# Optimization experiments

Hardware: AMD Instinct MI355X
Metric: run time of the kernel (lower is better)

The kernel has to match this reference:

```python
import jax, jax.numpy as jnp
import numpy as np

B, C, H, W = 16, 512, 64, 64


def setup_inputs() -> dict:
    key = jax.random.key(0)
    ks = jax.random.split(key, 8)
    s = 1.0 / np.sqrt(C)  # fan-in scale like torch conv default
    return {
        "x": jax.random.normal(ks[0], (B, C, H, W), dtype=jnp.float32),
        "y": jax.random.normal(ks[1], (B, C), dtype=jnp.float32),
        "wq": jax.random.normal(ks[2], (C, C), dtype=jnp.float32) * s,
        "bq": jax.random.normal(ks[3], (C,), dtype=jnp.float32) * s,
        "wk": jax.random.normal(ks[4], (C, C), dtype=jnp.float32) * s,
        "bk": jax.random.normal(ks[5], (C,), dtype=jnp.float32) * s,
        "wv": jax.random.normal(ks[6], (C, C), dtype=jnp.float32) * s,
        "bv": jax.random.normal(ks[7], (C,), dtype=jnp.float32) * s,
        "gamma": jnp.ones((1,), dtype=jnp.float32),
    }


def _conv1x1_flat(inp_flat, w, b):
    # inp_flat: (B, C, N); 1x1 conv == per-pixel channel GEMM
    return jnp.einsum("oc,bcn->bon", w, inp_flat) + b[None, :, None]


def reference(x, y, wq, bq, wk, bk, wv, bv, gamma):
    b, c, h, w = x.shape
    n = h * w
    # align=True: y (B, C) broadcast to (B, C, H, W); flatten spatial dims
    y_flat = jnp.broadcast_to(y[:, :, None], (b, c, n))
    x_flat = x.reshape(b, c, n)
    # exchange=False: q = y, k = v = x
    pq = _conv1x1_flat(y_flat, wq, bq)          # (B, C, N)
    pk = _conv1x1_flat(x_flat, wk, bk)          # (B, C, N)
    pv = _conv1x1_flat(x_flat, wv, bv)          # (B, C, N)
    energy = jnp.einsum("bcn,bdn->bcd", pq, pk)  # (B, C, C) channel attention
    attn = jax.nn.softmax(energy, axis=-1)
    out = jnp.einsum("bcd,bdn->bcn", attn, pv)   # (B, C, N)
    out = out.reshape(b, c, h, w)
    return gamma * out + x
```

## Files before the change

### kernel.cpp

```cpp
#include <hip/hip_runtime.h>
#include <hip/hip_bf16.h>

#define Bn 16
#define Cn 512
#define Nn 4096

typedef unsigned short u16;
typedef __bf16 bf16x8 __attribute__((ext_vector_type(8)));
typedef float f32x4 __attribute__((ext_vector_type(4)));

__device__ __forceinline__ u16 f2bf(float f) {
    __hip_bfloat16 h = __float2bfloat16(f);
    return *reinterpret_cast<u16*>(&h);
}

__global__ __launch_bounds__(256) void k_transpose(
    const float* __restrict__ x, u16* __restrict__ xt, float* __restrict__ sxp)
{
    __shared__ float tile[64 * 65];
    const int b = blockIdx.z, c0 = blockIdx.y * 64, n0 = blockIdx.x * 64;
    const int t = threadIdx.x;
    const float* xb = x + ((size_t)(b * Cn + c0)) * Nn + n0;

    float part[4];
#pragma unroll
    for (int r = 0; r < 4; ++r) {
        int cl = (t >> 4) + r * 16;
        int nl = (t & 15) * 4;
        float4 v = *(const float4*)(xb + (size_t)cl * Nn + nl);
        float* tp = &tile[cl * 65 + nl];
        tp[0] = v.x; tp[1] = v.y; tp[2] = v.z; tp[3] = v.w;
        part[r] = (v.x + v.y) + (v.z + v.w);
    }
#pragma unroll
    for (int m = 1; m < 16; m <<= 1) {
#pragma unroll
        for (int r = 0; r < 4; ++r) part[r] += __shfl_xor(part[r], m);
    }
    if ((t & 15) == 0) {
#pragma unroll
        for (int r = 0; r < 4; ++r) {
            int cl = (t >> 4) + r * 16;
            sxp[(size_t)(b * Cn + c0 + cl) * 64 + blockIdx.x] = part[r];
        }
    }
    __syncthreads();
    u16* xtb = xt + ((size_t)(b * Nn + n0)) * Cn + c0;
#pragma unroll
    for (int r = 0; r < 4; ++r) {
        int nl = (t >> 4) + r * 16;
        int c4 = (t & 15) * 4;
        ushort4 h;
        h.x = f2bf(tile[(c4 + 0) * 65 + nl]);
        h.y = f2bf(tile[(c4 + 1) * 65 + nl]);
        h.z = f2bf(tile[(c4 + 2) * 65 + nl]);
        h.w = f2bf(tile[(c4 + 3) * 65 + nl]);
        *(ushort4*)(xtb + (size_t)nl * Cn + c4) = h;
    }
}

__global__ __launch_bounds__(256) void k_sxred(
    const float* __restrict__ sxp, float* __restrict__ sx)
{
    int i = blockIdx.x * 256 + threadIdx.x;
    const float* p = sxp + (size_t)i * 64;
    float s = 0.f;
#pragma unroll
    for (int j = 0; j < 64; ++j) s += p[j];
    sx[i] = s;
}

__global__ __launch_bounds__(256) void k_qk(
    const float* __restrict__ wq, const float* __restrict__ bq,
    const float* __restrict__ wk, const float* __restrict__ bk,
    const float* __restrict__ y, const float* __restrict__ sx,
    float* __restrict__ qy, float* __restrict__ sk)
{
    const int w = threadIdx.x >> 6, lane = threadIdx.x & 63;
    const int o = blockIdx.x * 4 + w;
    const int b = blockIdx.y;
    const int mode = blockIdx.z;
    const float* W = mode ? wk : wq;
    const float* vec = mode ? (sx + b * Cn) : (y + b * Cn);
    float sum = 0.f;
#pragma unroll
    for (int i = 0; i < 8; ++i) {
        int k2 = lane + i * 64;
        sum += W[(size_t)o * Cn + k2] * vec[k2];
    }
#pragma unroll
    for (int m = 1; m < 64; m <<= 1) sum += __shfl_xor(sum, m);
    if (lane == 0) {
        if (mode) sk[b * Cn + o] = sum + 4096.0f * bk[o];
        else      qy[b * Cn + o] = sum + bq[o];
    }
}

__global__ __launch_bounds__(256) void k_wvt(
    const float* __restrict__ wv, u16* __restrict__ wvt)
{
    int idx = blockIdx.x * 256 + threadIdx.x;
    int e = idx >> 9, d = idx & 511;
    wvt[idx] = f2bf(wv[(size_t)d * Cn + e]);
}

__global__ __launch_bounds__(256) void k_softmax(
    const float* __restrict__ qy, const float* __restrict__ sk,
    const float* __restrict__ bv, u16* __restrict__ attn,
    float* __restrict__ beff)
{
    __shared__ float red[4], red2[4], red3[4];
    const int b = blockIdx.x >> 9, c = blockIdx.x & 511;
    const int t = threadIdx.x;
    const float q = qy[b * Cn + c];
    const float l0 = q * sk[b * Cn + t];
    const float l1 = q * sk[b * Cn + t + 256];
    float mx = fmaxf(l0, l1);
#pragma unroll
    for (int m = 1; m < 64; m <<= 1) mx = fmaxf(mx, __shfl_xor(mx, m));
    if ((t & 63) == 0) red[t >> 6] = mx;
    __syncthreads();
    mx = fmaxf(fmaxf(red[0], red[1]), fmaxf(red[2], red[3]));
    const float e0 = __expf(l0 - mx), e1 = __expf(l1 - mx);
    float s = e0 + e1;
#pragma unroll
    for (int m = 1; m < 64; m <<= 1) s += __shfl_xor(s, m);
    if ((t & 63) == 0) red2[t >> 6] = s;
    __syncthreads();
    s = red2[0] + red2[1] + red2[2] + red2[3];
    const float inv = 1.0f / s;
    const float a0 = e0 * inv, a1 = e1 * inv;
    u16* arow = attn + ((size_t)(b * Cn + c)) * Cn;
    arow[t] = f2bf(a0);
    arow[t + 256] = f2bf(a1);
    float pb = a0 * bv[t] + a1 * bv[t + 256];
#pragma unroll
    for (int m = 1; m < 64; m <<= 1) pb += __shfl_xor(pb, m);
    if ((t & 63) == 0) red3[t >> 6] = pb;
    __syncthreads();
    if (t == 0) beff[b * Cn + c] = red3[0] + red3[1] + red3[2] + red3[3];
}

template <int FINAL>
__global__ __launch_bounds__(256) void k_gemm(
    const u16* __restrict__ A, size_t strideA,
    const u16* __restrict__ Bt, size_t strideB,
    int N,
    u16* __restrict__ outBf, size_t strideOb,
    float* __restrict__ outF,
    const float* __restrict__ xres,
    const float* __restrict__ beff,
    const float* __restrict__ gamma)
{
    constexpr int K = 512;
    __shared__ u16 la[128 * 32];
    __shared__ u16 lb[128 * 32];
    const int b = blockIdx.z;
    const int m0 = blockIdx.y * 128;
    const int n0 = blockIdx.x * 128;
    A  += (size_t)b * strideA;
    Bt += (size_t)b * strideB;
    const int t = threadIdx.x;
    const int lane = t & 63;
    const int w = t >> 6;
    const int wm = (w >> 1) * 64, wn = (w & 1) * 64;
    const int l15 = lane & 15, quad = lane >> 4;

    f32x4 acc[4][4];
#pragma unroll
    for (int i = 0; i < 4; ++i)
#pragma unroll
        for (int j = 0; j < 4; ++j)
            acc[i][j] = (f32x4){0.f, 0.f, 0.f, 0.f};

    const int srow = t >> 2;
    const int scol = (t & 3) * 8;

    for (int k0 = 0; k0 < K; k0 += 32) {
        __syncthreads();
        *(uint4*)&la[srow * 32 + scol] =
            *(const uint4*)(A + (size_t)(m0 + srow) * K + k0 + scol);
        *(uint4*)&la[(srow + 64) * 32 + scol] =
            *(const uint4*)(A + (size_t)(m0 + srow + 64) * K + k0 + scol);
        *(uint4*)&lb[srow * 32 + scol] =
            *(const uint4*)(Bt + (size_t)(n0 + srow) * K + k0 + scol);
        *(uint4*)&lb[(srow + 64) * 32 + scol] =
            *(const uint4*)(Bt + (size_t)(n0 + srow + 64) * K + k0 + scol);
        __syncthreads();

        bf16x8 af[4], bfr[4];
#pragma unroll
        for (int mi = 0; mi < 4; ++mi)
            af[mi] = *(const bf16x8*)&la[(wm + mi * 16 + l15) * 32 + quad * 8];
#pragma unroll
        for (int ni = 0; ni < 4; ++ni)
            bfr[ni] = *(const bf16x8*)&lb[(wn + ni * 16 + l15) * 32 + quad * 8];
#pragma unroll
        for (int mi = 0; mi < 4; ++mi)
#pragma unroll
            for (int ni = 0; ni < 4; ++ni)
                acc[mi][ni] = __builtin_amdgcn_mfma_f32_16x16x32_bf16(
                    af[mi], bfr[ni], acc[mi][ni], 0, 0, 0);
    }

    if (FINAL) {
        const float g = gamma[0];
#pragma unroll
        for (int mi = 0; mi < 4; ++mi) {
#pragma unroll
            for (int reg = 0; reg < 4; ++reg) {
                const int r = m0 + wm + mi * 16 + quad * 4 + reg;
                const float be = beff[b * Cn + r];
                const size_t base = ((size_t)(b * Cn + r)) * N;
#pragma unroll
                for (int ni = 0; ni < 4; ++ni) {
                    const int cidx = n0 + wn + ni * 16 + l15;
                    outF[base + cidx] = g * (acc[mi][ni][reg] + be) + xres[base + cidx];
                }
            }
        }
    } else {
#pragma unroll
        for (int mi = 0; mi < 4; ++mi) {
#pragma unroll
            for (int reg = 0; reg < 4; ++reg) {
                const int r = m0 + wm + mi * 16 + quad * 4 + reg;
                const size_t base = (size_t)b * strideOb + (size_t)r * N;
#pragma unroll
                for (int ni = 0; ni < 4; ++ni) {
                    const int cidx = n0 + wn + ni * 16 + l15;
                    outBf[base + cidx] = f2bf(acc[mi][ni][reg]);
                }
            }
        }
    }
}

extern "C" void kernel_launch(void* const* d_in, const int* in_sizes, int n_in,
                              void* d_out, int out_size, void* d_ws, size_t ws_size,
                              hipStream_t stream)
{
    const float* x     = (const float*)d_in[0];
    const float* y     = (const float*)d_in[1];
    const float* wq    = (const float*)d_in[2];
    const float* bq    = (const float*)d_in[3];
    const float* wk    = (const float*)d_in[4];
    const float* bk    = (const float*)d_in[5];
    const float* wv    = (const float*)d_in[6];
    const float* bv    = (const float*)d_in[7];
    const float* gamma = (const float*)d_in[8];
    float* out = (float*)d_out;

    char* ws = (char*)d_ws;
    u16*   xt   = (u16*)  (ws + 0);
    float* sxp  = (float*)(ws + 67108864);
    float* sx   = (float*)(ws + 69206016);
    float* qy   = (float*)(ws + 69238784);
    float* sk   = (float*)(ws + 69271552);
    float* beff = (float*)(ws + 69304320);
    u16*   attn = (u16*)  (ws + 69337088);
    u16*   wvt  = (u16*)  (ws + 77725696);
    u16*   weff = (u16*)  (ws + 78249984);

    k_transpose<<<dim3(64, 8, Bn), dim3(256), 0, stream>>>(x, xt, sxp);
    k_sxred<<<dim3(32), dim3(256), 0, stream>>>(sxp, sx);
    k_wvt<<<dim3(1024), dim3(256), 0, stream>>>(wv, wvt);
    k_qk<<<dim3(128, Bn, 2), dim3(256), 0, stream>>>(wq, bq, wk, bk, y, sx, qy, sk);
    k_softmax<<<dim3(Bn * Cn), dim3(256), 0, stream>>>(qy, sk, bv, attn, beff);
    k_gemm<0><<<dim3(4, 4, Bn), dim3(256), 0, stream>>>(
        attn, (size_t)Cn * Cn, wvt, (size_t)0, Cn,
        weff, (size_t)Cn * Cn, nullptr, nullptr, nullptr, nullptr);
    k_gemm<1><<<dim3(32, 4, Bn), dim3(256), 0, stream>>>(
        weff, (size_t)Cn * Cn, xt, (size_t)Nn * Cn, Nn,
        nullptr, (size_t)0, out, x, beff, gamma);
}
```

Before: 366.4 us.

## Use direct global-to-LDS loads in GEMM and widen transpose writes

GEMM tile staging now uses global_load_lds so each wave copies its 16-row slice of A and B straight into shared memory, with no register round trip. The x transpose handles 128 channels per block and writes 16-byte bf16 vectors. The wv transpose becomes an LDS-tiled, coalesced kernel, and the partial-sum reduction reads float4. Together these aim to cut load-issue overhead and uncoalesced memory traffic, at the cost of more LDS use per transpose block.

Result: no change. 361.1 us (-1.4%).

```diff
diff --git a/kernel.cpp b/kernel.cpp
--- a/kernel.cpp
+++ b/kernel.cpp
@@ -8,23 +8,30 @@
 typedef unsigned short u16;
 typedef __bf16 bf16x8 __attribute__((ext_vector_type(8)));
 typedef float f32x4 __attribute__((ext_vector_type(4)));
+typedef unsigned short u16x8 __attribute__((ext_vector_type(8)));
 
 __device__ __forceinline__ u16 f2bf(float f) {
     __hip_bfloat16 h = __float2bfloat16(f);
     return *reinterpret_cast<u16*>(&h);
 }
 
+__device__ __forceinline__ void glds16(const u16* g, u16* l) {
+    __builtin_amdgcn_global_load_lds(
+        (const __attribute__((address_space(1))) void*)g,
+        (__attribute__((address_space(3))) void*)l, 16, 0, 0);
+}
+
 __global__ __launch_bounds__(256) void k_transpose(
     const float* __restrict__ x, u16* __restrict__ xt, float* __restrict__ sxp)
 {
-    __shared__ float tile[64 * 65];
-    const int b = blockIdx.z, c0 = blockIdx.y * 64, n0 = blockIdx.x * 64;
+    __shared__ float tile[128 * 65];
+    const int b = blockIdx.z, c0 = blockIdx.y * 128, n0 = blockIdx.x * 64;
     const int t = threadIdx.x;
     const float* xb = x + ((size_t)(b * Cn + c0)) * Nn + n0;
 
-    float part[4];
-#pragma unroll
-    for (int r = 0; r < 4; ++r) {
+    float part[8];
+#pragma unroll
+    for (int r = 0; r < 8; ++r) {
         int cl = (t >> 4) + r * 16;
         int nl = (t & 15) * 4;
         float4 v = *(const float4*)(xb + (size_t)cl * Nn + nl);
@@ -35,11 +42,11 @@
 #pragma unroll
     for (int m = 1; m < 16; m <<= 1) {
 #pragma unroll
-        for (int r = 0; r < 4; ++r) part[r] += __shfl_xor(part[r], m);
+        for (int r = 0; r < 8; ++r) part[r] += __shfl_xor(part[r], m);
     }
     if ((t & 15) == 0) {
 #pragma unroll
-        for (int r = 0; r < 4; ++r) {
+        for (int r = 0; r < 8; ++r) {
             int cl = (t >> 4) + r * 16;
             sxp[(size_t)(b * Cn + c0 + cl) * 64 + blockIdx.x] = part[r];
         }
@@ -49,13 +56,11 @@
 #pragma unroll
     for (int r = 0; r < 4; ++r) {
         int nl = (t >> 4) + r * 16;
-        int c4 = (t & 15) * 4;
-        ushort4 h;
-        h.x = f2bf(tile[(c4 + 0) * 65 + nl]);
-        h.y = f2bf(tile[(c4 + 1) * 65 + nl]);
-        h.z = f2bf(tile[(c4 + 2) * 65 + nl]);
-        h.w = f2bf(tile[(c4 + 3) * 65 + nl]);
-        *(ushort4*)(xtb + (size_t)nl * Cn + c4) = h;
+        int c8 = (t & 15) * 8;
+        u16x8 hv;
+#pragma unroll
+        for (int i = 0; i < 8; ++i) hv[i] = f2bf(tile[(c8 + i) * 65 + nl]);
+        *(u16x8*)(xtb + (size_t)nl * Cn + c8) = hv;
     }
 }
 
@@ -63,10 +68,13 @@
     const float* __restrict__ sxp, float* __restrict__ sx)
 {
     int i = blockIdx.x * 256 + threadIdx.x;
-    const float* p = sxp + (size_t)i * 64;
+    const float4* p = (const float4*)(sxp + (size_t)i * 64);
     float s = 0.f;
 #pragma unroll
-    for (int j = 0; j < 64; ++j) s += p[j];
+    for (int j = 0; j < 16; ++j) {
+        float4 v = p[j];
+        s += (v.x + v.y) + (v.z + v.w);
+    }
     sx[i] = s;
 }
 
@@ -99,9 +107,27 @@
 __global__ __launch_bounds__(256) void k_wvt(
     const float* __restrict__ wv, u16* __restrict__ wvt)
 {
-    int idx = blockIdx.x * 256 + threadIdx.x;
-    int e = idx >> 9, d = idx & 511;
-    wvt[idx] = f2bf(wv[(size_t)d * Cn + e]);
+    __shared__ float tl[64 * 65];
+    const int d0 = blockIdx.x * 64, e0 = blockIdx.y * 64;
+    const int t = threadIdx.x;
+#pragma unroll
+    for (int r = 0; r < 4; ++r) {
+        int d = (t >> 4) + r * 16, e4 = (t & 15) * 4;
+        float4 v = *(const float4*)(wv + (size_t)(d0 + d) * Cn + e0 + e4);
+        float* p = &tl[d * 65 + e4];
+        p[0] = v.x; p[1] = v.y; p[2] = v.z; p[3] = v.w;
+    }
+    __syncthreads();
+#pragma unroll
+    for (int r = 0; r < 4; ++r) {
+        int e = (t >> 4) + r * 16, d4 = (t & 15) * 4;
+        ushort4 h;
+        h.x = f2bf(tl[(d4 + 0) * 65 + e]);
+        h.y = f2bf(tl[(d4 + 1) * 65 + e]);
+        h.z = f2bf(tl[(d4 + 2) * 65 + e]);
+        h.w = f2bf(tl[(d4 + 3) * 65 + e]);
+        *(ushort4*)(wvt + (size_t)(e0 + e) * Cn + d0 + d4) = h;
+    }
 }
 
 __global__ __launch_bounds__(256) void k_softmax(
@@ -173,19 +199,18 @@
         for (int j = 0; j < 4; ++j)
             acc[i][j] = (f32x4){0.f, 0.f, 0.f, 0.f};
 
-    const int srow = t >> 2;
-    const int scol = (t & 3) * 8;
+    const int rb = w * 16;
+    const int lrow = lane >> 2;
+    const int lcol = (lane & 3) * 8;
 
     for (int k0 = 0; k0 < K; k0 += 32) {
         __syncthreads();
-        *(uint4*)&la[srow * 32 + scol] =
-            *(const uint4*)(A + (size_t)(m0 + srow) * K + k0 + scol);
-        *(uint4*)&la[(srow + 64) * 32 + scol] =
-            *(const uint4*)(A + (size_t)(m0 + srow + 64) * K + k0 + scol);
-        *(uint4*)&lb[srow * 32 + scol] =
-            *(const uint4*)(Bt + (size_t)(n0 + srow) * K + k0 + scol);
-        *(uint4*)&lb[(srow + 64) * 32 + scol] =
-            *(const uint4*)(Bt + (size_t)(n0 + srow + 64) * K + k0 + scol);
+        const u16* gA = A + (size_t)(m0 + rb + lrow) * K + k0 + lcol;
+        glds16(gA, &la[rb * 32]);
+        glds16(gA + (size_t)64 * K, &la[(rb + 64) * 32]);
+        const u16* gB = Bt + (size_t)(n0 + rb + lrow) * K + k0 + lcol;
+        glds16(gB, &lb[rb * 32]);
+        glds16(gB + (size_t)64 * K, &lb[(rb + 64) * 32]);
         __syncthreads();
 
         bf16x8 af[4], bfr[4];
@@ -262,9 +287,9 @@
     u16*   wvt  = (u16*)  (ws + 77725696);
     u16*   weff = (u16*)  (ws + 78249984);
 
-    k_transpose<<<dim3(64, 8, Bn), dim3(256), 0, stream>>>(x, xt, sxp);
+    k_transpose<<<dim3(64, 4, Bn), dim3(256), 0, stream>>>(x, xt, sxp);
     k_sxred<<<dim3(32), dim3(256), 0, stream>>>(sxp, sx);
-    k_wvt<<<dim3(1024), dim3(256), 0, stream>>>(wv, wvt);
+    k_wvt<<<dim3(8, 8), dim3(256), 0, stream>>>(wv, wvt);
     k_qk<<<dim3(128, Bn, 2), dim3(256), 0, stream>>>(wq, bq, wk, bk, y, sx, qy, sk);
     k_softmax<<<dim3(Bn * Cn), dim3(256), 0, stream>>>(qy, sk, bv, attn, beff);
     k_gemm<0><<<dim3(4, 4, Bn), dim3(256), 0, stream>>>(
```
